# Performance work log

Measured on AMD Instinct MI355X. Metric: run time of the kernel, lower is better.

## Reference

```python
import jax, jax.numpy as jnp
import numpy as np
import math

B, T, C = 8, 2048, 1024
KEY_SIZE, VALUE_SIZE = 1024, 1024


def setup_inputs() -> dict:
    key = jax.random.key(0)
    ks = jax.random.split(key, 7)
    s = 1.0 / math.sqrt(C)
    return {
        "input": jax.random.normal(ks[0], (B, T, C), dtype=jnp.float32),
        "mask": jnp.ones((B, T, 1), dtype=jnp.float32),
        "Wq": jax.random.uniform(ks[1], (C, KEY_SIZE), jnp.float32, -s, s),
        "bq": jax.random.uniform(ks[2], (KEY_SIZE,), jnp.float32, -s, s),
        "Wk": jax.random.uniform(ks[3], (C, KEY_SIZE), jnp.float32, -s, s),
        "bk": jax.random.uniform(ks[4], (KEY_SIZE,), jnp.float32, -s, s),
        "Wv": jax.random.uniform(ks[5], (C, VALUE_SIZE), jnp.float32, -s, s),
        "bv": jax.random.uniform(ks[6], (VALUE_SIZE,), jnp.float32, -s, s),
    }


def reference(input, mask, Wq, bq, Wk, bk, Wv, bv):
    # QKV projections: [B, T, C] @ [C, K] -> [B, T, K]
    query = input @ Wq + bq
    keys = input @ Wk + bk
    values = input @ Wv + bv
    # scores[b, tq, tk] = query[b, tq, :] . keys[b, tk, :]
    scores = jnp.einsum("bqk,btk->bqt", query, keys) / math.sqrt(KEY_SIZE)
    # NOTE: softmax over the QUERY dimension (axis=1), as in the original (dim=1)
    attn = jax.nn.softmax(scores, axis=1)
    out = jnp.einsum("bqt,btv->bqv", attn, values)
    return out * mask
```

## Files before the change

kernel.cpp:

```cpp
#include <hip/hip_runtime.h>
#include <hip/hip_bf16.h>
#include <cstdint>

typedef __attribute__((ext_vector_type(8))) __bf16 bf16x8;
typedef __attribute__((ext_vector_type(4))) float f32x4;
typedef __attribute__((ext_vector_type(8))) unsigned short u16x8;

static __device__ __forceinline__ unsigned short f2b(float f) {
    union { float f; unsigned u; } v; v.f = f;
    unsigned r = v.u + 0x7fffu + ((v.u >> 16) & 1u);
    return (unsigned short)(r >> 16);
}
static __device__ __forceinline__ float b2f(unsigned short b) {
    union { unsigned u; float f; } v; v.u = ((unsigned)b) << 16;
    return v.f;
}

#define LL16(g, l) __builtin_amdgcn_global_load_lds( \
    (const __attribute__((address_space(1))) void*)(g), \
    (__attribute__((address_space(3))) void*)(l), 16, 0, 0)

#define BAR() __builtin_amdgcn_s_barrier()
#define WAIT_VM0() asm volatile("s_waitcnt vmcnt(0)" ::: "memory")

__global__ void conv_f32_bf16(const float* __restrict__ in,
                              unsigned short* __restrict__ out, long n8) {
    long i = (long)blockIdx.x * blockDim.x + threadIdx.x;
    if (i >= n8) return;
    const float4* p = (const float4*)in + i * 2;
    float4 a = p[0], b = p[1];
    u16x8 r;
    r[0] = f2b(a.x); r[1] = f2b(a.y); r[2] = f2b(a.z); r[3] = f2b(a.w);
    r[4] = f2b(b.x); r[5] = f2b(b.y); r[6] = f2b(b.z); r[7] = f2b(b.w);
    *(u16x8*)(out + i * 8) = r;
}

__global__ void conv_x(const float* __restrict__ in,
                       unsigned short* __restrict__ out,
                       const float* __restrict__ wqbk,
                       const float* __restrict__ wkbq,
                       float* __restrict__ u, float* __restrict__ v) {
    long i = (long)blockIdx.x * blockDim.x + threadIdx.x;
    const float4* p = (const float4*)in + i * 2;
    float4 a = p[0], b = p[1];
    u16x8 r;
    r[0] = f2b(a.x); r[1] = f2b(a.y); r[2] = f2b(a.z); r[3] = f2b(a.w);
    r[4] = f2b(b.x); r[5] = f2b(b.y); r[6] = f2b(b.z); r[7] = f2b(b.w);
    *(u16x8*)(out + i * 8) = r;
    const int c = (int)(i & 127) * 8;
    const long row = i >> 7;
    const float* wq = wqbk + c;
    const float* wk = wkbq + c;
    float du = a.x*wq[0] + a.y*wq[1] + a.z*wq[2] + a.w*wq[3]
             + b.x*wq[4] + b.y*wq[5] + b.z*wq[6] + b.w*wq[7];
    float dv = a.x*wk[0] + a.y*wk[1] + a.z*wk[2] + a.w*wk[3]
             + b.x*wk[4] + b.y*wk[5] + b.z*wk[6] + b.w*wk[7];
    #pragma unroll
    for (int s = 1; s < 64; s <<= 1) {
        du += __shfl_xor(du, s);
        dv += __shfl_xor(dv, s);
    }
    if ((threadIdx.x & 63) == 0) {
        atomicAdd(&u[row], du);
        atomicAdd(&v[row], dv);
    }
}

__global__ void wdots(const float* __restrict__ Wq, const float* __restrict__ bq,
                      const float* __restrict__ Wk, const float* __restrict__ bk,
                      float* __restrict__ wqbk, float* __restrict__ wkbq,
                      float* __restrict__ cbuf) {
    const int lane = threadIdx.x & 63;
    if (blockIdx.x == 256) {
        float s = 0.f;
        for (int k = threadIdx.x; k < 1024; k += 256) s += bq[k] * bk[k];
        #pragma unroll
        for (int sh = 1; sh < 64; sh <<= 1) s += __shfl_xor(s, sh);
        __shared__ float ps[4];
        if (lane == 0) ps[threadIdx.x >> 6] = s;
        __syncthreads();
        if (threadIdx.x == 0) cbuf[0] = ps[0] + ps[1] + ps[2] + ps[3];
        return;
    }
    const int c = blockIdx.x * 4 + (threadIdx.x >> 6);
    const float* wq = Wq + (long)c * 1024;
    const float* wk = Wk + (long)c * 1024;
    float sq = 0.f, sk = 0.f;
    for (int k0 = 0; k0 < 1024; k0 += 256) {
        int k = k0 + lane * 4;
        float4 q4 = *(const float4*)(wq + k);
        float4 k4 = *(const float4*)(wk + k);
        float4 b4 = *(const float4*)(bk + k);
        float4 a4 = *(const float4*)(bq + k);
        sq += q4.x*b4.x + q4.y*b4.y + q4.z*b4.z + q4.w*b4.w;
        sk += k4.x*a4.x + k4.y*a4.y + k4.z*a4.z + k4.w*a4.w;
    }
    #pragma unroll
    for (int sh = 1; sh < 64; sh <<= 1) {
        sq += __shfl_xor(sq, sh);
        sk += __shfl_xor(sk, sh);
    }
    if (lane == 0) { wqbk[c] = sq; wkbq[c] = sk; }
}

__global__ void transpose_wv(const float* __restrict__ W,
                             unsigned short* __restrict__ out) {
    __shared__ float tile[32][33];
    int n0 = blockIdx.x * 32, c0 = blockIdx.y * 32;
    int tx = threadIdx.x & 31, ty = threadIdx.x >> 5;
    #pragma unroll
    for (int i = 0; i < 32; i += 8)
        tile[ty + i][tx] = W[(long)(c0 + ty + i) * 1024 + n0 + tx];
    __syncthreads();
    #pragma unroll
    for (int i = 0; i < 32; i += 8)
        out[(long)(n0 + ty + i) * 1024 + c0 + tx] = f2b(tile[tx][ty + i]);
}

__global__ void scale_vt(unsigned short* __restrict__ Vt,
                         const float* __restrict__ colsum) {
    long i8 = ((long)blockIdx.x * 256 + threadIdx.x) * 8;
    int b = (int)(i8 >> 21);
    int rem = (int)(i8 & ((1 << 21) - 1));
    int t = rem & 2047;
    const float* cs = colsum + b * 2048 + t;
    u16x8 v = *(const u16x8*)(Vt + i8);
    u16x8 o;
    #pragma unroll
    for (int j = 0; j < 8; ++j) o[j] = f2b(b2f(v[j]) / cs[j]);
    *(u16x8*)(Vt + i8) = o;
}


template<int MODE>
__global__ __launch_bounds__(256, 3)
void gemm128(const unsigned short* __restrict__ Aall,
             const unsigned short* __restrict__ Ball,
             void* __restrict__ Cv,
             int M, int N, int K, int ldc,
             long aStride, long bStride, long cStride,
             const float* __restrict__ aux, float* __restrict__ colsum) {
    __shared__ unsigned short lds[16384];

    const int gx = gridDim.x, gy = gridDim.y;
    const int nxy = gx * gy;
    const int nwg = nxy * gridDim.z;
    const int orig = (blockIdx.z * gy + blockIdx.y) * gx + blockIdx.x;
    const int swz = (orig & 7) * (nwg >> 3) + (orig >> 3);
    const int bz = swz / nxy;
    const int rem = swz - bz * nxy;
    const int sb = rem / (gy * 4);
    const int r2 = rem - sb * (gy * 4);
    const int by = r2 >> 2;
    const int bx = sb * 4 + (r2 & 3);

    const unsigned short* A  = Aall + (long)bz * aStride;
    const unsigned short* Bt = Ball + (long)bz * bStride;

    const int tid = threadIdx.x;
    const int lane = tid & 63;
    const int w = tid >> 6;
    const int wrow = w >> 1, wcol = w & 1;
    const int lr = lane & 15, lg = lane >> 4;

    const int bm = by * 128, bn = bx * 128;
    const int NT = K >> 6;

    const int r0 = tid >> 3;
    const int c0 = (tid & 7) ^ (r0 & 7);
    const unsigned short* sA = A  + (long)(bm + r0) * K + c0 * 8;
    const unsigned short* sB = Bt + (long)(bn + r0) * K + c0 * 8;
    const long R32 = 32L * K;
    const int dstT = tid * 8;

    const int cx0 = (lg ^ (lr & 7)) * 8;
    const int cx1 = ((4 + lg) ^ (lr & 7)) * 8;
    const int baA = (wrow * 64 + lr) * 64;
    const int baB = 8192 + (wcol * 64 + lr) * 64;

    f32x4 acc[4][4] = {};

    for (int t = 0; t < NT; ++t) {
        const long ko = (long)t * 64;
        LL16(sA + ko,            lds + dstT);
        LL16(sA + ko + R32,      lds + 2048 + dstT);
        LL16(sA + ko + 2 * R32,  lds + 4096 + dstT);
        LL16(sA + ko + 3 * R32,  lds + 6144 + dstT);
        LL16(sB + ko,            lds + 8192 + dstT);
        LL16(sB + ko + R32,      lds + 10240 + dstT);
        LL16(sB + ko + 2 * R32,  lds + 12288 + dstT);
        LL16(sB + ko + 3 * R32,  lds + 14336 + dstT);
        WAIT_VM0();
        BAR();

        bf16x8 bf[4][2];
        #pragma unroll
        for (int nj = 0; nj < 4; ++nj) {
            bf[nj][0] = *(const bf16x8*)(lds + baB + nj * 1024 + cx0);
            bf[nj][1] = *(const bf16x8*)(lds + baB + nj * 1024 + cx1);
        }
        __builtin_amdgcn_s_setprio(1);
        #pragma unroll
        for (int mi = 0; mi < 4; ++mi) {
            bf16x8 a0 = *(const bf16x8*)(lds + baA + mi * 1024 + cx0);
            bf16x8 a1 = *(const bf16x8*)(lds + baA + mi * 1024 + cx1);
            #pragma unroll
            for (int nj = 0; nj < 4; ++nj) {
                acc[mi][nj] = __builtin_amdgcn_mfma_f32_16x16x32_bf16(
                    a0, bf[nj][0], acc[mi][nj], 0, 0, 0);
                acc[mi][nj] = __builtin_amdgcn_mfma_f32_16x16x32_bf16(
                    a1, bf[nj][1], acc[mi][nj], 0, 0, 0);
            }
        }
        __builtin_amdgcn_s_setprio(0);

        BAR();
    }

    if (MODE != 3) {
        unsigned short* C = (unsigned short*)Cv + (long)bz * cStride;
        float* cs = colsum + (long)bz * 2048;
        const float cQK = (MODE == 2) ? aux[32768] : 0.f;
        #pragma unroll
        for (int h = 0; h < 2; ++h) {
            if (h) BAR();
            if (wrow == h) {
                #pragma unroll
                for (int nj = 0; nj < 4; ++nj) {
                    const int cl = wcol * 64 + nj * 16 + lr;
                    const int cb = cl >> 3, cIn = cl & 7;
                    float vcol = (MODE == 2) ? (aux[16384 + bz * 2048 + bn + cl] + cQK) : 0.f;
                    float psum = 0.f;
                    #pragma unroll
                    for (int mi = 0; mi < 4; ++mi) {
                        #pragma unroll
                        for (int r = 0; r < 4; ++r) {
                            const int rl = mi * 16 + lg * 4 + r;
                            float val = acc[mi][nj][r];
                            if (MODE == 1) val += aux[bm + h * 64 + rl];
                            else if (MODE == 2) {
                                val = __expf((val + aux[bz * 2048 + bm + h * 64 + rl] + vcol) * 0.03125f);
                                psum += val;
                            }
                            lds[rl * 128 + ((cb ^ ((rl & 7) << 1)) << 3) + cIn] = f2b(val);
                        }
                    }
                    if (MODE == 2) {
                        psum += __shfl_xor(psum, 16);
                        psum += __shfl_xor(psum, 32);
                        if (lg == 0) atomicAdd(&cs[bn + cl], psum);
                    }
                }
            }
            BAR();
            #pragma unroll
            for (int it = 0; it < 4; ++it) {
                int lin = it * 256 + tid;
                int row = lin >> 4;
                int c = lin & 15;
                u16x8 v = *(const u16x8*)&lds[row * 128 + ((c ^ ((row & 7) << 1)) << 3)];
                *(u16x8*)&C[(long)(bm + h * 64 + row) * ldc + bn + c * 8] = v;
            }
        }
    } else {
        float* C = (float*)Cv + (long)bz * cStride;
        const float* mk = aux + (long)bz * 2048;
        float* ft = (float*)lds;
        #pragma unroll
        for (int q = 0; q < 4; ++q) {
            if (q) BAR();
            if (wrow == (q >> 1)) {
                const int mlo = (q & 1) * 2;
                #pragma unroll
                for (int nj = 0; nj < 4; ++nj) {
                    const int cl = wcol * 64 + nj * 16 + lr;
                    const int cf = cl >> 2, cIn = cl & 3;
                    #pragma unroll
                    for (int mi = 0; mi < 2; ++mi) {
                        #pragma unroll
                        for (int r = 0; r < 4; ++r) {
                            const int rl = mi * 16 + lg * 4 + r;
                            const int gr = bm + q * 32 + rl;
                            ft[rl * 128 + ((cf ^ ((rl & 7) << 2)) << 2) + cIn] =
                                acc[mlo + mi][nj][r] * mk[gr];
                        }
                    }
                }
            }
            BAR();
            #pragma unroll
            for (int it = 0; it < 4; ++it) {
                int lin = it * 256 + tid;
                int row = lin >> 5;
                int cf = lin & 31;
                float4 v = *(const float4*)&ft[row * 128 + ((cf ^ ((row & 7) << 2)) << 2)];
                *(float4*)&C[(long)(bm + q * 32 + row) * ldc + bn + cf * 4] = v;
            }
        }
    }
}

extern "C" void kernel_launch(void* const* d_in, const int* in_sizes, int n_in,
                              void* d_out, int out_size, void* d_ws, size_t ws_size,
                              hipStream_t stream) {
    const float* x    = (const float*)d_in[0];
    const float* mask = (const float*)d_in[1];
    const float* Wq   = (const float*)d_in[2];
    const float* bq   = (const float*)d_in[3];
    const float* Wk   = (const float*)d_in[4];
    const float* bk   = (const float*)d_in[5];
    const float* Wv   = (const float*)d_in[6];
    const float* bv   = (const float*)d_in[7];
    float* out = (float*)d_out;

    const long MT = 16384;
    unsigned short* Xb  = (unsigned short*)d_ws;
    unsigned short* Wqb = Xb + MT * 1024;
    unsigned short* Wkb = Wqb + 1048576;
    unsigned short* Wvt = Wkb + 1048576;
    unsigned short* Y   = Wvt + 1048576;
    unsigned short* Z   = Y + MT * 1024;
    unsigned short* Vt  = Z + MT * 1024;
    unsigned short* E   = Vt + 8L * 1024 * 2048;
    float* colsum = (float*)(E + 8L * 2048 * 2048);
    float* u      = colsum + 16384;
    float* v      = u + 16384;
    float* cbuf   = v + 16384;
    float* wqbk   = cbuf + 1;
    float* wkbq   = wqbk + 1024;
    size_t need = (size_t)((char*)(wkbq + 1024) - (char*)d_ws);
    if (ws_size < need) return;

    hipMemsetAsync(colsum, 0, 3L * 16384 * sizeof(float), stream);
    wdots<<<257, 256, 0, stream>>>(Wq, bq, Wk, bk, wqbk, wkbq, cbuf);
    conv_x<<<8192, 256, 0, stream>>>(x, Xb, wqbk, wkbq, u, v);
    conv_f32_bf16<<<512, 256, 0, stream>>>(Wq, Wqb, 131072);
    conv_f32_bf16<<<512, 256, 0, stream>>>(Wk, Wkb, 131072);
    transpose_wv<<<dim3(32, 32), 256, 0, stream>>>(Wv, Wvt);
    gemm128<0><<<dim3(8, 8, 1), 256, 0, stream>>>(
        Wkb, Wqb, Z, 1024, 1024, 1024, 1024, 0, 0, 0, nullptr, nullptr);
    gemm128<0><<<dim3(8, 128, 1), 256, 0, stream>>>(
        Xb, Z, Y, 16384, 1024, 1024, 1024, 0, 0, 0, nullptr, nullptr);
    gemm128<1><<<dim3(16, 8, 8), 256, 0, stream>>>(
        Wvt, Xb, Vt, 1024, 2048, 1024, 2048,
        0, 2048L * 1024, 1024L * 2048, bv, nullptr);
    gemm128<2><<<dim3(16, 16, 8), 256, 0, stream>>>(
        Y, Xb, E, 2048, 2048, 1024, 2048,
        2048L * 1024, 2048L * 1024, 2048L * 2048, u, colsum);
    scale_vt<<<8192, 256, 0, stream>>>(Vt, colsum);
    gemm128<3><<<dim3(8, 16, 8), 256, 0, stream>>>(
        E, Vt, out, 2048, 1024, 2048, 1024,
        2048L * 2048, 1024L * 2048, 2048L * 1024, mask, nullptr);
}
```

Baseline: 343.2 us.

## Double-buffer GEMM K-tiles with async LDS prefetch and merge weight conversions

The GEMM main loop changes from a single 64-wide K tile loaded and fully waited each iteration to two 32-wide K buffers in the same LDS space. The next tile is prefetched while the current one is computed, using a partial vmcnt wait, so global-to-LDS latency overlaps with MFMA work. Launch bounds rise to 4 waves-per-SIMD occupancy. The two weight conversion launches are merged into one 2D launch. The trade-off is twice as many barriers per K and less MFMA work per barrier, plus possible register pressure from the higher occupancy target.

Measured after the change: 342.7 us. Within noise of the previous version (-0.2%).

```diff
diff --git a/kernel.cpp b/kernel.cpp
--- a/kernel.cpp
+++ b/kernel.cpp
@@ -21,18 +21,21 @@
     (__attribute__((address_space(3))) void*)(l), 16, 0, 0)
 
 #define BAR() __builtin_amdgcn_s_barrier()
+#define WAIT_VM4() asm volatile("s_waitcnt vmcnt(4)" ::: "memory")
 #define WAIT_VM0() asm volatile("s_waitcnt vmcnt(0)" ::: "memory")
 
-__global__ void conv_f32_bf16(const float* __restrict__ in,
-                              unsigned short* __restrict__ out, long n8) {
+__global__ void conv_w2(const float* __restrict__ w0,
+                        const float* __restrict__ w1,
+                        unsigned short* __restrict__ out) {
     long i = (long)blockIdx.x * blockDim.x + threadIdx.x;
-    if (i >= n8) return;
+    const float* in = blockIdx.y ? w1 : w0;
+    unsigned short* o = out + (long)blockIdx.y * 1048576;
     const float4* p = (const float4*)in + i * 2;
     float4 a = p[0], b = p[1];
     u16x8 r;
     r[0] = f2b(a.x); r[1] = f2b(a.y); r[2] = f2b(a.z); r[3] = f2b(a.w);
     r[4] = f2b(b.x); r[5] = f2b(b.y); r[6] = f2b(b.z); r[7] = f2b(b.w);
-    *(u16x8*)(out + i * 8) = r;
+    *(u16x8*)(o + i * 8) = r;
 }
 
 __global__ void conv_x(const float* __restrict__ in,
@@ -133,7 +136,7 @@
 
 
 template<int MODE>
-__global__ __launch_bounds__(256, 3)
+__global__ __launch_bounds__(256, 4)
 void gemm128(const unsigned short* __restrict__ Aall,
              const unsigned short* __restrict__ Ball,
              void* __restrict__ Cv,
@@ -164,58 +167,54 @@
     const int lr = lane & 15, lg = lane >> 4;
 
     const int bm = by * 128, bn = bx * 128;
-    const int NT = K >> 6;
-
-    const int r0 = tid >> 3;
-    const int c0 = (tid & 7) ^ (r0 & 7);
+    const int NT = K >> 5;
+
+    const int r0 = tid >> 2;
+    const int c0 = (tid & 3) ^ (r0 & 3);
     const unsigned short* sA = A  + (long)(bm + r0) * K + c0 * 8;
     const unsigned short* sB = Bt + (long)(bn + r0) * K + c0 * 8;
-    const long R32 = 32L * K;
+    const long R64 = 64L * K;
     const int dstT = tid * 8;
 
-    const int cx0 = (lg ^ (lr & 7)) * 8;
-    const int cx1 = ((4 + lg) ^ (lr & 7)) * 8;
-    const int baA = (wrow * 64 + lr) * 64;
-    const int baB = 8192 + (wcol * 64 + lr) * 64;
+    const int cx0 = (lg ^ (lr & 3)) * 8;
+    const int baA = (wrow * 64 + lr) * 32 + cx0;
+    const int baB = 8192 + (wcol * 64 + lr) * 32 + cx0;
 
     f32x4 acc[4][4] = {};
 
+    #define STAGE(kt, buf) do { const long ko = (long)(kt) * 32; \
+        LL16(sA + ko,       lds + (buf) * 4096 + dstT); \
+        LL16(sA + ko + R64, lds + (buf) * 4096 + 2048 + dstT); \
+        LL16(sB + ko,       lds + 8192 + (buf) * 4096 + dstT); \
+        LL16(sB + ko + R64, lds + 8192 + (buf) * 4096 + 2048 + dstT); } while (0)
+
+    STAGE(0, 0);
+    STAGE(1, 1);
+
     for (int t = 0; t < NT; ++t) {
-        const long ko = (long)t * 64;
-        LL16(sA + ko,            lds + dstT);
-        LL16(sA + ko + R32,      lds + 2048 + dstT);
-        LL16(sA + ko + 2 * R32,  lds + 4096 + dstT);
-        LL16(sA + ko + 3 * R32,  lds + 6144 + dstT);
-        LL16(sB + ko,            lds + 8192 + dstT);
-        LL16(sB + ko + R32,      lds + 10240 + dstT);
-        LL16(sB + ko + 2 * R32,  lds + 12288 + dstT);
-        LL16(sB + ko + 3 * R32,  lds + 14336 + dstT);
-        WAIT_VM0();
+        if (t < NT - 1) { WAIT_VM4(); } else { WAIT_VM0(); }
         BAR();
 
-        bf16x8 bf[4][2];
-        #pragma unroll
-        for (int nj = 0; nj < 4; ++nj) {
-            bf[nj][0] = *(const bf16x8*)(lds + baB + nj * 1024 + cx0);
-            bf[nj][1] = *(const bf16x8*)(lds + baB + nj * 1024 + cx1);
-        }
+        const int bb = (t & 1) * 4096;
+        bf16x8 bf[4];
+        #pragma unroll
+        for (int nj = 0; nj < 4; ++nj)
+            bf[nj] = *(const bf16x8*)(lds + bb + baB + nj * 512);
         __builtin_amdgcn_s_setprio(1);
         #pragma unroll
         for (int mi = 0; mi < 4; ++mi) {
-            bf16x8 a0 = *(const bf16x8*)(lds + baA + mi * 1024 + cx0);
-            bf16x8 a1 = *(const bf16x8*)(lds + baA + mi * 1024 + cx1);
+            bf16x8 a0 = *(const bf16x8*)(lds + bb + baA + mi * 512);
             #pragma unroll
-            for (int nj = 0; nj < 4; ++nj) {
+            for (int nj = 0; nj < 4; ++nj)
                 acc[mi][nj] = __builtin_amdgcn_mfma_f32_16x16x32_bf16(
-                    a0, bf[nj][0], acc[mi][nj], 0, 0, 0);
-                acc[mi][nj] = __builtin_amdgcn_mfma_f32_16x16x32_bf16(
-                    a1, bf[nj][1], acc[mi][nj], 0, 0, 0);
-            }
+                    a0, bf[nj], acc[mi][nj], 0, 0, 0);
         }
         __builtin_amdgcn_s_setprio(0);
 
         BAR();
-    }
+        if (t + 2 < NT) STAGE(t + 2, t & 1);
+    }
+    #undef STAGE
 
     if (MODE != 3) {
         unsigned short* C = (unsigned short*)Cv + (long)bz * cStride;
@@ -334,8 +333,7 @@
     hipMemsetAsync(colsum, 0, 3L * 16384 * sizeof(float), stream);
     wdots<<<257, 256, 0, stream>>>(Wq, bq, Wk, bk, wqbk, wkbq, cbuf);
     conv_x<<<8192, 256, 0, stream>>>(x, Xb, wqbk, wkbq, u, v);
-    conv_f32_bf16<<<512, 256, 0, stream>>>(Wq, Wqb, 131072);
-    conv_f32_bf16<<<512, 256, 0, stream>>>(Wk, Wkb, 131072);
+    conv_w2<<<dim3(512, 2), 256, 0, stream>>>(Wq, Wk, Wqb);
     transpose_wv<<<dim3(32, 32), 256, 0, stream>>>(Wv, Wvt);
     gemm128<0><<<dim3(8, 8, 1), 256, 0, stream>>>(
         Wkb, Wqb, Z, 1024, 1024, 1024, 1024, 0, 0, 0, nullptr, nullptr);
```
